# Performance work log

Hardware: AMD Instinct MI355X
Metric: run time of the kernel (lower is better)

## Reference

```python
import jax, jax.numpy as jnp
import numpy as np

N_NODES = 50000
N_EDGES = 800000


def _sage_conv(h, ei, W_l, W_r, b_l):
    """PyG SAGEConv: lin_l(mean_{j->i} h_j) + lin_r(h_i). lin_l has bias, lin_r does not."""
    src, dst = ei[0], ei[1]
    # mean-aggregate raw features first (linear commutes with mean) to avoid [E, out] intermediates
    msum = jax.ops.segment_sum(h[src], dst, num_segments=N_NODES)          # [N, d]
    cnt = jax.ops.segment_sum(jnp.ones((ei.shape[1], 1), h.dtype), dst,
                              num_segments=N_NODES)                         # [N, 1]
    mean = msum / jnp.maximum(cnt, 1.0)
    return mean @ W_l + b_l + h @ W_r


def setup_inputs() -> dict:
    key = jax.random.key(0)
    ks = jax.random.split(key, 8)
    d_in, d_hid, d_out = 64, 64, 32
    return {
        "x": jax.random.normal(ks[0], (N_NODES, d_in), dtype=jnp.float32),
        "ei0": jax.random.randint(ks[1], (2, N_EDGES), 0, N_NODES, dtype=jnp.int32),
        "ei1": jax.random.randint(ks[2], (2, N_EDGES), 0, N_NODES, dtype=jnp.int32),
        "Wl": jax.random.normal(ks[3], (2, 2, d_in, d_hid), dtype=jnp.float32) * 0.05,
        "Wr": jax.random.normal(ks[4], (2, 2, d_in, d_hid), dtype=jnp.float32) * 0.05,
        "bl": jax.random.normal(ks[5], (2, 2, d_hid), dtype=jnp.float32) * 0.05,
        "lin_W": jax.random.normal(ks[6], (d_hid, d_out), dtype=jnp.float32) * 0.05,
        "lin_b": jax.random.normal(ks[7], (d_out,), dtype=jnp.float32) * 0.05,
    }


def reference(x, ei0, ei1, Wl, Wr, bl, lin_W, lin_b):
    edge_indices = (ei0, ei1)  # one edge_index per relation
    h = x
    for l in range(2):  # layers (structurally fixed)
        out = None
        for r, ei in enumerate(edge_indices):  # HeteroConv aggr='sum' over relations
            y = _sage_conv(h, ei, Wl[l, r], Wr[l, r], bl[l, r])
            out = y if out is None else out + y
        h = jax.nn.relu(out)
    return h @ lin_W + lin_b
```

## Files before the change

### kernel.cpp

```cpp
#include <hip/hip_runtime.h>

#define NN 50000
#define CAP 32
#define OVF_CAP 4096
#define SHARD_W 6250
#define NSH 8
#define NCH 128

__device__ __forceinline__ unsigned short f2bf(float f) {
    unsigned u = __float_as_uint(f);
    u += 0x7fffu + ((u >> 16) & 1u);
    return (unsigned short)(u >> 16);
}
__device__ __forceinline__ float bf2f(unsigned short u) {
    return __uint_as_float(((unsigned)u) << 16);
}

__global__ __launch_bounds__(256) void init_fuse(
    const float* __restrict__ in, unsigned short* __restrict__ out, int n4,
    int* __restrict__ zbuf, int nint)
{
    int stride = gridDim.x * blockDim.x;
    int id0 = blockIdx.x * blockDim.x + threadIdx.x;
    for (int i = id0; i < n4; i += stride) {
        float4 v = ((const float4*)in)[i];
        ushort4 o;
        o.x = f2bf(v.x); o.y = f2bf(v.y); o.z = f2bf(v.z); o.w = f2bf(v.w);
        ((ushort4*)out)[i] = o;
    }
    for (int i = id0; i < nint; i += stride) zbuf[i] = 0;
}


__global__ __launch_bounds__(256, 6) void count_pass(
    const int* __restrict__ ei0, int E0,
    const int* __restrict__ ei1, int E1,
    unsigned char* __restrict__ cnt)
{
    __shared__ unsigned int lcnt32[SHARD_W / 2];
    int q   = blockIdx.x & (NSH - 1);
    int c   = (blockIdx.x >> 3) & (NCH - 1);
    int rel = blockIdx.x >> 10;
    const int* ei = rel ? ei1 : ei0;
    int E         = rel ? E1  : E0;
    int ce = (E + NCH - 1) / NCH;
    int lo = c * ce;
    int hi = min(lo + ce, E);
    int nlo = q * SHARD_W;

    for (int i = threadIdx.x; i < SHARD_W / 2; i += 256) lcnt32[i] = 0;
    __syncthreads();
    for (int t = lo + threadIdx.x; t < hi; t += 256) {
        int loc = ei[E + t] - nlo;
        if ((unsigned)loc < (unsigned)SHARD_W)
            atomicAdd(&lcnt32[loc >> 1], 1u << ((loc & 1) << 4));
    }
    __syncthreads();
    unsigned short* dst =
        (unsigned short*)(cnt + ((size_t)(rel * NCH + c)) * NN + nlo);
    for (int i = threadIdx.x; i < SHARD_W / 2; i += 256) {
        unsigned w = lcnt32[i];
        unsigned a = min(w & 0xffffu, 255u);
        unsigned b = min(w >> 16, 255u);
        dst[i] = (unsigned short)(a | (b << 8));
    }
}

__global__ __launch_bounds__(256) void prefix_pass(
    const unsigned char* __restrict__ cnt,
    unsigned char* __restrict__ bases,
    int* __restrict__ deg)
{
    int t = blockIdx.x * 256 + threadIdx.x;
    if (t >= 2 * (NN / 4)) return;
    int rel = t / (NN / 4);
    int n4  = (t % (NN / 4)) * 4;

    unsigned run0 = 0, run1 = 0, run2 = 0, run3 = 0;
    #pragma unroll 4
    for (int c = 0; c < NCH; c++) {
        size_t idx = ((size_t)(rel * NCH + c)) * NN + n4;
        unsigned v = *(const unsigned*)&cnt[idx];
        unsigned b0 = min(run0, 255u), b1 = min(run1, 255u);
        unsigned b2 = min(run2, 255u), b3 = min(run3, 255u);
        *(unsigned*)&bases[idx] = b0 | (b1 << 8) | (b2 << 16) | (b3 << 24);
        run0 += v & 255u;
        run1 += (v >> 8) & 255u;
        run2 += (v >> 16) & 255u;
        run3 += (v >> 24);
    }
    *(int4*)&deg[rel * NN + n4] = make_int4(run0, run1, run2, run3);
}

__global__ __launch_bounds__(256, 6) void place_pass(
    const int* __restrict__ ei0, int E0,
    const int* __restrict__ ei1, int E1,
    const unsigned char* __restrict__ bases,
    unsigned short* __restrict__ bins,
    int2* __restrict__ ovf, int* __restrict__ ovf_cnt)
{
    __shared__ unsigned int lcnt32[SHARD_W / 2];
    __shared__ unsigned short lbase16[SHARD_W / 2];
    int q   = blockIdx.x & (NSH - 1);
    int c   = (blockIdx.x >> 3) & (NCH - 1);
    int rel = blockIdx.x >> 10;
    const int* ei = rel ? ei1 : ei0;
    int E         = rel ? E1  : E0;
    int ce = (E + NCH - 1) / NCH;
    int lo = c * ce;
    int hi = min(lo + ce, E);
    int nlo = q * SHARD_W;

    const unsigned short* bsrc =
        (const unsigned short*)(bases + ((size_t)(rel * NCH + c)) * NN + nlo);
    for (int i = threadIdx.x; i < SHARD_W / 2; i += 256) {
        lbase16[i] = bsrc[i];
        lcnt32[i] = 0;
    }
    __syncthreads();

    int taskbase = rel * NN + nlo;
    for (int t = lo + threadIdx.x; t < hi; t += 256) {
        int loc = ei[E + t] - nlo;
        if ((unsigned)loc < (unsigned)SHARD_W) {
            int s = ei[t];
            int sh = (loc & 1) << 4;
            unsigned r32 = atomicAdd(&lcnt32[loc >> 1], 1u << sh);
            int r = (int)((r32 >> sh) & 0xffffu);
            int b = (int)((lbase16[loc >> 1] >> ((loc & 1) << 3)) & 0xffu);
            int slot = b + r;
            int task = taskbase + loc;
            if (slot < CAP) {
                bins[(size_t)task * CAP + slot] = (unsigned short)s;
            } else {
                int o = atomicAdd(ovf_cnt, 1);
                if (o < OVF_CAP) ovf[o] = make_int2(task, s);
            }
        }
    }
}

__global__ __launch_bounds__(256) void aggregate(
    const unsigned short* __restrict__ bins, const int* __restrict__ deg,
    const unsigned short* __restrict__ hb, unsigned short* __restrict__ agg,
    const int2* __restrict__ ovf, const int* __restrict__ ovf_cnt)
{
    int lane = threadIdx.x & 63;
    int half = lane >> 5;
    int p = lane & 31;
    int wid = (blockIdx.x * blockDim.x + threadIdx.x) >> 6;
    int nwaves = (gridDim.x * blockDim.x) >> 6;
    const unsigned int* hb32 = (const unsigned int*)hb;
    unsigned int* agg32 = (unsigned int*)agg;

    for (int task = wid; task < 2 * NN; task += nwaves) {
        int d = deg[task];
        int m = min(d, CAP);
        int idx = 0;
        if (lane < m) idx = bins[(size_t)task * CAP + lane];
        float a00=0.f,a01=0.f, a10=0.f,a11=0.f, a20=0.f,a21=0.f, a30=0.f,a31=0.f;
        int F = m >> 1;
        int q = 0;
        for (; q + 4 <= F; q += 4) {
            int s0 = __shfl(idx, 2*(q+0) + half);
            int s1 = __shfl(idx, 2*(q+1) + half);
            int s2 = __shfl(idx, 2*(q+2) + half);
            int s3 = __shfl(idx, 2*(q+3) + half);
            unsigned u0 = hb32[(size_t)s0 * 32 + p];
            unsigned u1 = hb32[(size_t)s1 * 32 + p];
            unsigned u2 = hb32[(size_t)s2 * 32 + p];
            unsigned u3 = hb32[(size_t)s3 * 32 + p];
            a00 += __uint_as_float(u0 << 16); a01 += __uint_as_float(u0 & 0xffff0000u);
            a10 += __uint_as_float(u1 << 16); a11 += __uint_as_float(u1 & 0xffff0000u);
            a20 += __uint_as_float(u2 << 16); a21 += __uint_as_float(u2 & 0xffff0000u);
            a30 += __uint_as_float(u3 << 16); a31 += __uint_as_float(u3 & 0xffff0000u);
        }
        for (; q < F; ++q) {
            int s = __shfl(idx, 2*q + half);
            unsigned u = hb32[(size_t)s * 32 + p];
            a00 += __uint_as_float(u << 16); a01 += __uint_as_float(u & 0xffff0000u);
        }
        if (m & 1) {
            int s = __shfl(idx, m - 1);
            if (half == 0) {
                unsigned u = hb32[(size_t)s * 32 + p];
                a00 += __uint_as_float(u << 16); a01 += __uint_as_float(u & 0xffff0000u);
            }
        }
        if (d > CAP) {
            int cnt = min(*ovf_cnt, OVF_CAP);
            for (int e = 0; e < cnt; ++e) {
                int2 v = ovf[e];
                if (v.x == task && half == 0) {
                    unsigned u = hb32[(size_t)v.y * 32 + p];
                    a00 += __uint_as_float(u << 16); a01 += __uint_as_float(u & 0xffff0000u);
                }
            }
        }
        float s0 = (a00 + a10) + (a20 + a30);
        float s1 = (a01 + a11) + (a21 + a31);
        s0 += __shfl_xor(s0, 32);
        s1 += __shfl_xor(s1, 32);
        if (half == 0) {
            float inv = 1.0f / (float)max(d, 1);
            unsigned lo = (unsigned)f2bf(s0 * inv);
            unsigned hi = (unsigned)f2bf(s1 * inv);
            agg32[(size_t)task * 32 + p] = lo | (hi << 16);
        }
    }
}

#define RST 132
__global__ __launch_bounds__(256) void layer_gemm(
    const unsigned short* __restrict__ agg0, const unsigned short* __restrict__ agg1,
    const unsigned short* __restrict__ selfb,
    const float* __restrict__ Wl0, const float* __restrict__ Wl1,
    const float* __restrict__ Wr0, const float* __restrict__ Wr1,
    const float* __restrict__ b0, const float* __restrict__ b1,
    unsigned short* __restrict__ hb16)
{
    __shared__ float Wch[64 * 64];
    __shared__ float rowsT[64 * RST];
    __shared__ float bias[64];

    int tid = threadIdx.x;
    int base = blockIdx.x * 128;
    if (tid < 64) bias[tid] = b0[tid] + b1[tid];

    int j8 = (tid & 7) * 8;
    int n4 = (tid >> 3) * 4;

    float acc[4][8];
    #pragma unroll
    for (int i = 0; i < 4; i++)
        #pragma unroll
        for (int c = 0; c < 8; c++) acc[i][c] = 0.f;

    for (int chunk = 0; chunk < 3; chunk++) {
        const float* W = (chunk == 0) ? Wl0 : (chunk == 1) ? Wl1 : Wr0;
        const unsigned short* src = (chunk == 0) ? agg0 : (chunk == 1) ? agg1 : selfb;
        __syncthreads();
        #pragma unroll
        for (int r = 0; r < 4; r++) {
            int i = tid + 256 * r;
            float4 w = *(const float4*)&W[i * 4];
            if (chunk == 2) {
                float4 w2 = *(const float4*)&Wr1[i * 4];
                w.x += w2.x; w.y += w2.y; w.z += w2.z; w.w += w2.w;
            }
            *(float4*)&Wch[i * 4] = w;
        }
        #pragma unroll
        for (int r = 0; r < 8; r++) {
            int i = tid + 256 * r;
            int node = i >> 4;
            int k4 = (i & 15) * 4;
            int g = base + node;
            ushort4 u = make_ushort4(0, 0, 0, 0);
            if (g < NN) u = *(const ushort4*)&src[(size_t)g * 64 + k4];
            rowsT[(k4 + 0) * RST + node] = bf2f(u.x);
            rowsT[(k4 + 1) * RST + node] = bf2f(u.y);
            rowsT[(k4 + 2) * RST + node] = bf2f(u.z);
            rowsT[(k4 + 3) * RST + node] = bf2f(u.w);
        }
        __syncthreads();
        #pragma unroll 4
        for (int k = 0; k < 64; k++) {
            float4 wa = *(const float4*)&Wch[k * 64 + j8];
            float4 wb = *(const float4*)&Wch[k * 64 + j8 + 4];
            float4 rv = *(const float4*)&rowsT[k * RST + n4];
            float w[8] = {wa.x, wa.y, wa.z, wa.w, wb.x, wb.y, wb.z, wb.w};
            float rr[4] = {rv.x, rv.y, rv.z, rv.w};
            #pragma unroll
            for (int i = 0; i < 4; i++)
                #pragma unroll
                for (int c = 0; c < 8; c++)
                    acc[i][c] = fmaf(rr[i], w[c], acc[i][c]);
        }
    }

    #pragma unroll
    for (int i = 0; i < 4; i++) {
        int g = base + n4 + i;
        if (g < NN) {
            ushort4 p0, p1;
            p0.x = f2bf(fmaxf(acc[i][0] + bias[j8 + 0], 0.f));
            p0.y = f2bf(fmaxf(acc[i][1] + bias[j8 + 1], 0.f));
            p0.z = f2bf(fmaxf(acc[i][2] + bias[j8 + 2], 0.f));
            p0.w = f2bf(fmaxf(acc[i][3] + bias[j8 + 3], 0.f));
            p1.x = f2bf(fmaxf(acc[i][4] + bias[j8 + 4], 0.f));
            p1.y = f2bf(fmaxf(acc[i][5] + bias[j8 + 5], 0.f));
            p1.z = f2bf(fmaxf(acc[i][6] + bias[j8 + 6], 0.f));
            p1.w = f2bf(fmaxf(acc[i][7] + bias[j8 + 7], 0.f));
            *(ushort4*)&hb16[(size_t)g * 64 + j8]     = p0;
            *(ushort4*)&hb16[(size_t)g * 64 + j8 + 4] = p1;
        }
    }
}

__global__ __launch_bounds__(256) void layer_gemm_final(
    const unsigned short* __restrict__ agg0, const unsigned short* __restrict__ agg1,
    const unsigned short* __restrict__ selfb,
    const float* __restrict__ Wl0, const float* __restrict__ Wl1,
    const float* __restrict__ Wr0, const float* __restrict__ Wr1,
    const float* __restrict__ b0, const float* __restrict__ b1,
    const float* __restrict__ linW, const float* __restrict__ linb,
    float* __restrict__ out)
{
    __shared__ float Wch[64 * 64];
    __shared__ float rowsT[64 * RST];
    __shared__ float bias[64];

    int tid = threadIdx.x;
    int base = blockIdx.x * 128;
    if (tid < 64) bias[tid] = b0[tid] + b1[tid];

    int j8 = (tid & 7) * 8;
    int n4 = (tid >> 3) * 4;

    float acc[4][8];
    #pragma unroll
    for (int i = 0; i < 4; i++)
        #pragma unroll
        for (int c = 0; c < 8; c++) acc[i][c] = 0.f;

    for (int chunk = 0; chunk < 3; chunk++) {
        const float* W = (chunk == 0) ? Wl0 : (chunk == 1) ? Wl1 : Wr0;
        const unsigned short* src = (chunk == 0) ? agg0 : (chunk == 1) ? agg1 : selfb;
        __syncthreads();
        #pragma unroll
        for (int r = 0; r < 4; r++) {
            int i = tid + 256 * r;
            float4 w = *(const float4*)&W[i * 4];
            if (chunk == 2) {
                float4 w2 = *(const float4*)&Wr1[i * 4];
                w.x += w2.x; w.y += w2.y; w.z += w2.z; w.w += w2.w;
            }
            *(float4*)&Wch[i * 4] = w;
        }
        #pragma unroll
        for (int r = 0; r < 8; r++) {
            int i = tid + 256 * r;
            int node = i >> 4;
            int k4 = (i & 15) * 4;
            int g = base + node;
            ushort4 u = make_ushort4(0, 0, 0, 0);
            if (g < NN) u = *(const ushort4*)&src[(size_t)g * 64 + k4];
            rowsT[(k4 + 0) * RST + node] = bf2f(u.x);
            rowsT[(k4 + 1) * RST + node] = bf2f(u.y);
            rowsT[(k4 + 2) * RST + node] = bf2f(u.z);
            rowsT[(k4 + 3) * RST + node] = bf2f(u.w);
        }
        __syncthreads();
        #pragma unroll 4
        for (int k = 0; k < 64; k++) {
            float4 wa = *(const float4*)&Wch[k * 64 + j8];
            float4 wb = *(const float4*)&Wch[k * 64 + j8 + 4];
            float4 rv = *(const float4*)&rowsT[k * RST + n4];
            float w[8] = {wa.x, wa.y, wa.z, wa.w, wb.x, wb.y, wb.z, wb.w};
            float rr[4] = {rv.x, rv.y, rv.z, rv.w};
            #pragma unroll
            for (int i = 0; i < 4; i++)
                #pragma unroll
                for (int c = 0; c < 8; c++)
                    acc[i][c] = fmaf(rr[i], w[c], acc[i][c]);
        }
    }

    float o[4][8];
    #pragma unroll
    for (int i = 0; i < 4; i++)
        #pragma unroll
        for (int c = 0; c < 8; c++)
            o[i][c] = fmaxf(acc[i][c] + bias[j8 + c], 0.f);

    __syncthreads();

    #pragma unroll
    for (int r = 0; r < 2; r++) {
        int i = tid + 256 * r;
        *(float4*)&Wch[i * 4] = *(const float4*)&linW[i * 4];
    }
    if (tid < 32) bias[tid] = linb[tid];
    #pragma unroll
    for (int i = 0; i < 4; i++)
        #pragma unroll
        for (int c = 0; c < 8; c++)
            rowsT[(j8 + c) * RST + (n4 + i)] = o[i][c];
    __syncthreads();

    int j4 = (tid & 7) * 4;
    float acc2[4][4];
    #pragma unroll
    for (int i = 0; i < 4; i++)
        #pragma unroll
        for (int c = 0; c < 4; c++) acc2[i][c] = 0.f;
    #pragma unroll 4
    for (int k = 0; k < 64; k++) {
        float4 w = *(const float4*)&Wch[k * 32 + j4];
        float4 rv = *(const float4*)&rowsT[k * RST + n4];
        float wr[4] = {w.x, w.y, w.z, w.w};
        float rr[4] = {rv.x, rv.y, rv.z, rv.w};
        #pragma unroll
        for (int i = 0; i < 4; i++)
            #pragma unroll
            for (int c = 0; c < 4; c++)
                acc2[i][c] = fmaf(rr[i], wr[c], acc2[i][c]);
    }
    #pragma unroll
    for (int i = 0; i < 4; i++) {
        int g = base + n4 + i;
        if (g < NN) {
            float4 ov;
            ov.x = acc2[i][0] + bias[j4 + 0];
            ov.y = acc2[i][1] + bias[j4 + 1];
            ov.z = acc2[i][2] + bias[j4 + 2];
            ov.w = acc2[i][3] + bias[j4 + 3];
            *(float4*)&out[(size_t)g * 32 + j4] = ov;
        }
    }
}

extern "C" void kernel_launch(void* const* d_in, const int* in_sizes, int n_in,
                              void* d_out, int out_size, void* d_ws, size_t ws_size,
                              hipStream_t stream)
{
    const float* x    = (const float*)d_in[0];
    const int*   ei0  = (const int*)d_in[1];
    const int*   ei1  = (const int*)d_in[2];
    const float* Wl   = (const float*)d_in[3];
    const float* Wr   = (const float*)d_in[4];
    const float* bl   = (const float*)d_in[5];
    const float* linW = (const float*)d_in[6];
    const float* linb = (const float*)d_in[7];
    float* out = (float*)d_out;

    int E0 = in_sizes[1] / 2;
    int E1 = in_sizes[2] / 2;

    unsigned short* bins = (unsigned short*)d_ws;
    unsigned short* h1b  = bins + (size_t)2 * NN * CAP;
    unsigned short* aggb = h1b + (size_t)NN * 64;
    unsigned short* agg0 = aggb;
    unsigned short* agg1 = aggb + (size_t)NN * 64;
    unsigned short* xb   = aggb + (size_t)2 * NN * 64;
    int*  deg     = (int*)(xb + (size_t)NN * 64);
    int*  ovf_cnt = deg + 2 * NN;
    int2* ovf     = (int2*)(ovf_cnt + 8);
    unsigned char* cnt   = (unsigned char*)bins;
    unsigned char* bases = (unsigned char*)aggb;

    dim3 blk(256);
    int ggrid = (NN + 127) / 128;

    init_fuse<<<1024, blk, 0, stream>>>(x, xb, NN * 16, ovf_cnt, 8);

    count_pass<<<2 * NCH * NSH, blk, 0, stream>>>(ei0, E0, ei1, E1, cnt);
    prefix_pass<<<(2 * (NN / 4) + 255) / 256, blk, 0, stream>>>(cnt, bases, deg);
    place_pass<<<2 * NCH * NSH, blk, 0, stream>>>(ei0, E0, ei1, E1, bases,
                                                  bins, ovf, ovf_cnt);

    aggregate<<<4096, blk, 0, stream>>>(bins, deg, xb, aggb, ovf, ovf_cnt);
    layer_gemm<<<ggrid, blk, 0, stream>>>(agg0, agg1, xb,
        Wl + 0, Wl + 4096, Wr + 0, Wr + 4096, bl + 0, bl + 64, h1b);

    aggregate<<<4096, blk, 0, stream>>>(bins, deg, h1b, aggb, ovf, ovf_cnt);
    layer_gemm_final<<<ggrid, blk, 0, stream>>>(agg0, agg1, h1b,
        Wl + 8192, Wl + 12288, Wr + 8192, Wr + 12288, bl + 128, bl + 192,
        linW, linb, out);
}
```

Measured before the change: 263.3 us.

## Replace chunk-by-shard edge binning with two-level radix partition by destination

Replaces the count/prefix/place passes, where every block scans its whole edge chunk and keeps only edges for one of 8 node shards, with a counting-sort style partition. Edges are bucketed into 782 shards of 64 nodes: a per-block shard histogram, per-shard totals, a global scan, per-block bases, then a partition into a compact array, and finally per-shard binning that also writes degrees. This removes the 8x redundant reads of the edge list and the large byte-count matrices. In exchange it adds more kernel launches, two serial loops over 512 blocks in the total and block-base passes, and a dependence on node ids fitting in 16 bits for the packed (dst,src) word. Within a node, bin slot order now follows atomic order rather than edge order.

```diff
diff --git a/kernel.cpp b/kernel.cpp
--- a/kernel.cpp
+++ b/kernel.cpp
@@ -3,9 +3,9 @@
 #define NN 50000
 #define CAP 32
 #define OVF_CAP 4096
-#define SHARD_W 6250
-#define NSH 8
-#define NCH 128
+#define SHARD_W 64
+#define NSH 782
+#define NPB 512
 
 __device__ __forceinline__ unsigned short f2bf(float f) {
     unsigned u = __float_as_uint(f);
@@ -32,111 +32,151 @@
 }
 
 
-__global__ __launch_bounds__(256, 6) void count_pass(
+__global__ __launch_bounds__(256) void shard_hist(
     const int* __restrict__ ei0, int E0,
     const int* __restrict__ ei1, int E1,
-    unsigned char* __restrict__ cnt)
-{
-    __shared__ unsigned int lcnt32[SHARD_W / 2];
-    int q   = blockIdx.x & (NSH - 1);
-    int c   = (blockIdx.x >> 3) & (NCH - 1);
-    int rel = blockIdx.x >> 10;
+    unsigned short* __restrict__ hist16)
+{
+    __shared__ unsigned lh[NSH];
+    int local = blockIdx.x; int rel = 0;
+    if (local >= NPB) { local -= NPB; rel = 1; }
+    int pb = (local & 7) * (NPB / 8) + (local >> 3);
     const int* ei = rel ? ei1 : ei0;
     int E         = rel ? E1  : E0;
-    int ce = (E + NCH - 1) / NCH;
-    int lo = c * ce;
-    int hi = min(lo + ce, E);
-    int nlo = q * SHARD_W;
-
-    for (int i = threadIdx.x; i < SHARD_W / 2; i += 256) lcnt32[i] = 0;
-    __syncthreads();
-    for (int t = lo + threadIdx.x; t < hi; t += 256) {
-        int loc = ei[E + t] - nlo;
-        if ((unsigned)loc < (unsigned)SHARD_W)
-            atomicAdd(&lcnt32[loc >> 1], 1u << ((loc & 1) << 4));
-    }
-    __syncthreads();
-    unsigned short* dst =
-        (unsigned short*)(cnt + ((size_t)(rel * NCH + c)) * NN + nlo);
-    for (int i = threadIdx.x; i < SHARD_W / 2; i += 256) {
-        unsigned w = lcnt32[i];
-        unsigned a = min(w & 0xffffu, 255u);
-        unsigned b = min(w >> 16, 255u);
-        dst[i] = (unsigned short)(a | (b << 8));
-    }
-}
-
-__global__ __launch_bounds__(256) void prefix_pass(
-    const unsigned char* __restrict__ cnt,
-    unsigned char* __restrict__ bases,
-    int* __restrict__ deg)
-{
-    int t = blockIdx.x * 256 + threadIdx.x;
-    if (t >= 2 * (NN / 4)) return;
-    int rel = t / (NN / 4);
-    int n4  = (t % (NN / 4)) * 4;
-
-    unsigned run0 = 0, run1 = 0, run2 = 0, run3 = 0;
-    #pragma unroll 4
-    for (int c = 0; c < NCH; c++) {
-        size_t idx = ((size_t)(rel * NCH + c)) * NN + n4;
-        unsigned v = *(const unsigned*)&cnt[idx];
-        unsigned b0 = min(run0, 255u), b1 = min(run1, 255u);
-        unsigned b2 = min(run2, 255u), b3 = min(run3, 255u);
-        *(unsigned*)&bases[idx] = b0 | (b1 << 8) | (b2 << 16) | (b3 << 24);
-        run0 += v & 255u;
-        run1 += (v >> 8) & 255u;
-        run2 += (v >> 16) & 255u;
-        run3 += (v >> 24);
-    }
-    *(int4*)&deg[rel * NN + n4] = make_int4(run0, run1, run2, run3);
-}
-
-__global__ __launch_bounds__(256, 6) void place_pass(
+    int ce = (E + NPB - 1) / NPB;
+    int lo = pb * ce, hi = min(lo + ce, E);
+
+    for (int i = threadIdx.x; i < NSH; i += 256) lh[i] = 0;
+    __syncthreads();
+    for (int t = lo + threadIdx.x; t < hi; t += 256)
+        atomicAdd(&lh[ei[E + t] >> 6], 1u);
+    __syncthreads();
+    unsigned short* row = hist16 + (size_t)(rel * NPB + pb) * NSH;
+    for (int i = threadIdx.x; i < NSH; i += 256)
+        row[i] = (unsigned short)lh[i];
+}
+
+__global__ __launch_bounds__(256) void total_pass(
+    const unsigned short* __restrict__ hist16, int* __restrict__ tot)
+{
+    int i = blockIdx.x * 256 + threadIdx.x;
+    if (i >= 2 * NSH) return;
+    int rel = i / NSH, s = i - rel * NSH;
+    int t = 0;
+    for (int b = 0; b < NPB; b++)
+        t += hist16[(size_t)(rel * NPB + b) * NSH + s];
+    tot[i] = t;
+}
+
+__global__ __launch_bounds__(256) void scan_pass(
+    const int* __restrict__ tot, int* __restrict__ sbase)
+{
+    __shared__ int ps[256];
+    int t = threadIdx.x;
+    int v[7];
+    int s = 0;
+    #pragma unroll
+    for (int j = 0; j < 7; j++) {
+        int i = t * 7 + j;
+        v[j] = (i < 2 * NSH) ? tot[i] : 0;
+        s += v[j];
+    }
+    ps[t] = s;
+    __syncthreads();
+    for (int off = 1; off < 256; off <<= 1) {
+        int add = (t >= off) ? ps[t - off] : 0;
+        __syncthreads();
+        ps[t] += add;
+        __syncthreads();
+    }
+    int run = (t == 0) ? 0 : ps[t - 1];
+    #pragma unroll
+    for (int j = 0; j < 7; j++) {
+        int i = t * 7 + j;
+        if (i < 2 * NSH) sbase[i] = run;
+        run += v[j];
+    }
+    if (t == 255) sbase[2 * NSH] = run;
+}
+
+__global__ __launch_bounds__(256) void blockbase_pass(
+    const unsigned short* __restrict__ hist16, const int* __restrict__ sbase,
+    unsigned* __restrict__ pbase)
+{
+    int i = blockIdx.x * 256 + threadIdx.x;
+    if (i >= 2 * NSH) return;
+    int rel = i / NSH, s = i - rel * NSH;
+    unsigned run = (unsigned)sbase[i];
+    for (int b = 0; b < NPB; b++) {
+        size_t idx = (size_t)(rel * NPB + b) * NSH + s;
+        pbase[idx] = run;
+        run += hist16[idx];
+    }
+}
+
+__global__ __launch_bounds__(256) void partition_pass(
     const int* __restrict__ ei0, int E0,
     const int* __restrict__ ei1, int E1,
-    const unsigned char* __restrict__ bases,
-    unsigned short* __restrict__ bins,
-    int2* __restrict__ ovf, int* __restrict__ ovf_cnt)
-{
-    __shared__ unsigned int lcnt32[SHARD_W / 2];
-    __shared__ unsigned short lbase16[SHARD_W / 2];
-    int q   = blockIdx.x & (NSH - 1);
-    int c   = (blockIdx.x >> 3) & (NCH - 1);
-    int rel = blockIdx.x >> 10;
+    const unsigned* __restrict__ pbase,
+    unsigned* __restrict__ compact)
+{
+    __shared__ unsigned lbase[NSH];
+    __shared__ unsigned lrank[NSH];
+    int local = blockIdx.x; int rel = 0;
+    if (local >= NPB) { local -= NPB; rel = 1; }
+    int pb = (local & 7) * (NPB / 8) + (local >> 3);
     const int* ei = rel ? ei1 : ei0;
     int E         = rel ? E1  : E0;
-    int ce = (E + NCH - 1) / NCH;
-    int lo = c * ce;
-    int hi = min(lo + ce, E);
-    int nlo = q * SHARD_W;
-
-    const unsigned short* bsrc =
-        (const unsigned short*)(bases + ((size_t)(rel * NCH + c)) * NN + nlo);
-    for (int i = threadIdx.x; i < SHARD_W / 2; i += 256) {
-        lbase16[i] = bsrc[i];
-        lcnt32[i] = 0;
-    }
-    __syncthreads();
-
-    int taskbase = rel * NN + nlo;
+    int ce = (E + NPB - 1) / NPB;
+    int lo = pb * ce, hi = min(lo + ce, E);
+
+    const unsigned* prow = pbase + (size_t)(rel * NPB + pb) * NSH;
+    for (int i = threadIdx.x; i < NSH; i += 256) {
+        lbase[i] = prow[i];
+        lrank[i] = 0;
+    }
+    __syncthreads();
     for (int t = lo + threadIdx.x; t < hi; t += 256) {
-        int loc = ei[E + t] - nlo;
-        if ((unsigned)loc < (unsigned)SHARD_W) {
-            int s = ei[t];
-            int sh = (loc & 1) << 4;
-            unsigned r32 = atomicAdd(&lcnt32[loc >> 1], 1u << sh);
-            int r = (int)((r32 >> sh) & 0xffffu);
-            int b = (int)((lbase16[loc >> 1] >> ((loc & 1) << 3)) & 0xffu);
-            int slot = b + r;
-            int task = taskbase + loc;
-            if (slot < CAP) {
-                bins[(size_t)task * CAP + slot] = (unsigned short)s;
-            } else {
-                int o = atomicAdd(ovf_cnt, 1);
-                if (o < OVF_CAP) ovf[o] = make_int2(task, s);
-            }
-        }
+        int dst = ei[E + t];
+        int src = ei[t];
+        int s = dst >> 6;
+        unsigned r = atomicAdd(&lrank[s], 1u);
+        compact[lbase[s] + r] = ((unsigned)dst << 16) | (unsigned)src;
+    }
+}
+
+__global__ __launch_bounds__(256) void bin_pass(
+    const unsigned* __restrict__ compact, const int* __restrict__ sbase,
+    unsigned short* __restrict__ bins, int* __restrict__ deg,
+    int2* __restrict__ ovf, int* __restrict__ ovf_cnt)
+{
+    __shared__ unsigned lcnt[SHARD_W];
+    int bid = blockIdx.x;
+    int rel = bid / NSH;
+    int s   = bid - rel * NSH;
+    if (threadIdx.x < SHARD_W) lcnt[threadIdx.x] = 0;
+    __syncthreads();
+    int base = sbase[bid];
+    int tot  = sbase[bid + 1] - base;
+    int taskbase = rel * NN + s * SHARD_W;
+    for (int j = threadIdx.x; j < tot; j += 256) {
+        unsigned e = compact[base + j];
+        int dst = (int)(e >> 16);
+        int src = (int)(e & 0xffffu);
+        int loc = dst & (SHARD_W - 1);
+        unsigned r = atomicAdd(&lcnt[loc], 1u);
+        int task = taskbase + loc;
+        if (r < CAP) {
+            bins[(size_t)task * CAP + r] = (unsigned short)src;
+        } else {
+            int o = atomicAdd(ovf_cnt, 1);
+            if (o < OVF_CAP) ovf[o] = make_int2(task, src);
+        }
+    }
+    __syncthreads();
+    if (threadIdx.x < SHARD_W) {
+        int node = s * SHARD_W + threadIdx.x;
+        if (node < NN) deg[rel * NN + node] = (int)lcnt[threadIdx.x];
     }
 }
 
@@ -447,18 +487,25 @@
     int*  deg     = (int*)(xb + (size_t)NN * 64);
     int*  ovf_cnt = deg + 2 * NN;
     int2* ovf     = (int2*)(ovf_cnt + 8);
-    unsigned char* cnt   = (unsigned char*)bins;
-    unsigned char* bases = (unsigned char*)aggb;
+
+    unsigned*       compact = (unsigned*)h1b;
+    unsigned short* hist16  = aggb;
+    unsigned*       pbase   = (unsigned*)(aggb + (size_t)2 * NPB * NSH);
+    int*            tot     = (int*)(aggb + (size_t)2 * NPB * NSH * 3);
+    int*            sbase   = tot + 2 * NSH;
 
     dim3 blk(256);
     int ggrid = (NN + 127) / 128;
+    int rows_grid = (2 * NSH + 255) / 256;
 
     init_fuse<<<1024, blk, 0, stream>>>(x, xb, NN * 16, ovf_cnt, 8);
 
-    count_pass<<<2 * NCH * NSH, blk, 0, stream>>>(ei0, E0, ei1, E1, cnt);
-    prefix_pass<<<(2 * (NN / 4) + 255) / 256, blk, 0, stream>>>(cnt, bases, deg);
-    place_pass<<<2 * NCH * NSH, blk, 0, stream>>>(ei0, E0, ei1, E1, bases,
-                                                  bins, ovf, ovf_cnt);
+    shard_hist<<<2 * NPB, blk, 0, stream>>>(ei0, E0, ei1, E1, hist16);
+    total_pass<<<rows_grid, blk, 0, stream>>>(hist16, tot);
+    scan_pass<<<1, blk, 0, stream>>>(tot, sbase);
+    blockbase_pass<<<rows_grid, blk, 0, stream>>>(hist16, sbase, pbase);
+    partition_pass<<<2 * NPB, blk, 0, stream>>>(ei0, E0, ei1, E1, pbase, compact);
+    bin_pass<<<2 * NSH, blk, 0, stream>>>(compact, sbase, bins, deg, ovf, ovf_cnt);
 
     aggregate<<<4096, blk, 0, stream>>>(bins, deg, xb, aggb, ovf, ovf_cnt);
     layer_gemm<<<ggrid, blk, 0, stream>>>(agg0, agg1, xb,
```

After: 297.6 us. 1.13x slower.
